# Kernel optimization log

Measured on AMD Instinct MI355X. Metric: run time of the kernel, lower is better.

The kernel has to match this reference:

```python
import jax, jax.numpy as jnp
import numpy as np

N = 50000      # nodes
E = 100000     # edges
F_NODE = 128
F_EDGE = 16
H = 64         # hidden_dim
OUT = 32
STEPS = 3
G = 64         # num_graphs (static; batch.max()+1 in torch)


def setup_inputs() -> dict:
    key = jax.random.key(0)
    ks = jax.random.split(key, 20)

    def lin(k, fin, fout):
        s = 1.0 / np.sqrt(fin)
        return jax.random.uniform(k, (fin, fout), jnp.float32, -s, s)

    def bias(k, fin, fout):
        s = 1.0 / np.sqrt(fin)
        return jax.random.uniform(k, (fout,), jnp.float32, -s, s)

    inp = {
        'x': jax.random.normal(ks[0], (N, F_NODE), jnp.float32),
        'edge_index': jax.random.randint(ks[1], (2, E), 0, N),
        'edge_attr': jax.random.normal(ks[2], (E, F_EDGE), jnp.float32),
        'batch': jnp.sort(jax.random.randint(ks[3], (N,), 0, G)),
        # node encoder
        'W_enc': lin(ks[4], F_NODE, H), 'b_enc': bias(ks[5], F_NODE, H),
        # edge_nn: Linear(F_EDGE,H) -> ReLU -> Linear(H, H*H)
        'W_e1': lin(ks[6], F_EDGE, H), 'b_e1': bias(ks[7], F_EDGE, H),
        'W_e2': lin(ks[8], H, H * H), 'b_e2': bias(ks[9], H, H * H),
        # GRUCell (torch layout: [3H, H])
        'W_ih': jax.random.uniform(ks[10], (3 * H, H), jnp.float32, -1/np.sqrt(H), 1/np.sqrt(H)),
        'W_hh': jax.random.uniform(ks[11], (3 * H, H), jnp.float32, -1/np.sqrt(H), 1/np.sqrt(H)),
        'b_ih': jax.random.uniform(ks[12], (3 * H,), jnp.float32, -1/np.sqrt(H), 1/np.sqrt(H)),
        'b_hh': jax.random.uniform(ks[13], (3 * H,), jnp.float32, -1/np.sqrt(H), 1/np.sqrt(H)),
        # readout MLP: Linear(H,H) -> ReLU -> Linear(H,OUT)
        'W_r1': lin(ks[14], H, H), 'b_r1': bias(ks[15], H, H),
        'W_r2': lin(ks[16], H, OUT), 'b_r2': bias(ks[17], H, OUT),
    }
    return inp


def gru_cell(m, h, W_ih, W_hh, b_ih, b_hh):
    gi = m @ W_ih.T + b_ih   # [N, 3H]
    gh = h @ W_hh.T + b_hh
    i_r, i_z, i_n = jnp.split(gi, 3, axis=-1)
    h_r, h_z, h_n = jnp.split(gh, 3, axis=-1)
    r = jax.nn.sigmoid(i_r + h_r)
    z = jax.nn.sigmoid(i_z + h_z)
    n = jnp.tanh(i_n + r * h_n)
    return (1.0 - z) * n + z * h


def reference(x, edge_index, edge_attr, batch, W_enc, b_enc, W_e1, b_e1,
              W_e2, b_e2, W_ih, W_hh, b_ih, b_hh, W_r1, b_r1, W_r2, b_r2):
    h = x @ W_enc + b_enc                                   # [N, H]
    src, dst = edge_index[0], edge_index[1]
    # edge-conditioned weight matrices (loop-invariant; compute once)
    ew = (jax.nn.relu(edge_attr @ W_e1 + b_e1) @ W_e2 + b_e2).reshape(E, H, H)
    for _ in range(STEPS):
        msg = jnp.einsum('eij,ej->ei', ew, h[src])          # per-edge matvec
        m_agg = jax.ops.segment_sum(msg, dst, num_segments=N)
        h = gru_cell(m_agg, h, W_ih, W_hh, b_ih, b_hh)
    g = jax.ops.segment_sum(h, batch, num_segments=G)       # sum readout
    return jax.nn.relu(g @ W_r1 + b_r1) @ W_r2 + b_r2
```

## Files before the change

kernel.cpp:

```cpp
#include <hip/hip_runtime.h>
#include <hip/hip_bf16.h>
#include <math.h>

#define NN 50000
#define NE 100000
#define FN 128
#define FE 16
#define HD 64
#define OUTD 32
#define NG 64
#define ZK 65

typedef unsigned int uint;
typedef unsigned short ushort;
typedef __attribute__((ext_vector_type(8))) short short8;
typedef __attribute__((ext_vector_type(16))) float f32x16;

static __device__ __forceinline__ float bfbits2f(uint u) {
    return __builtin_bit_cast(float, u << 16);
}
static __device__ __forceinline__ uint packbf(float f0, float f1) {
    return __builtin_amdgcn_perm(__builtin_bit_cast(uint, f1),
                                 __builtin_bit_cast(uint, f0), 0x07060302u);
}
static __device__ __forceinline__ ushort f2bf(float f) {
    uint u = __builtin_bit_cast(uint, f);
    u = (u + 0x7FFFu + ((u >> 16) & 1u)) >> 16;
    return (ushort)u;
}
static __device__ __forceinline__ uint pack2rne(float f0, float f1) {
    return (uint)f2bf(f0) | ((uint)f2bf(f1) << 16);
}
static __device__ __forceinline__ float fsigmoid(float x) {
    return 1.f / (1.f + __expf(-x));
}
static __device__ __forceinline__ float ftanh(float x) {
    float t = __expf(2.f * x);
    return 1.f - 2.f / (t + 1.f);
}

#define PREP_S0 (ZK * 4096)
#define PREP_S1 (256 * 128)
__global__ void k_prep(const float* __restrict__ W_e2, const float* __restrict__ b_e2,
                       const float* __restrict__ W_ih, const float* __restrict__ W_hh,
                       ushort* __restrict__ Wtb, ushort* __restrict__ Bg) {
    int idx = blockIdx.x * 256 + threadIdx.x;
    if (idx < PREP_S0) {
        int k0 = idx >> 12, r = idx & 4095;
        int jb = r >> 9, i = (r >> 3) & 63, q = r & 7;
        int j = jb * 8 + q;
        float v = (k0 < 64) ? W_e2[k0 * 4096 + i * 64 + j] : b_e2[i * 64 + j];
        Wtb[idx] = f2bf(v);
        return;
    }
    idx -= PREP_S0;
    if (idx < PREP_S1) {
        int n = idx >> 7, k = idx & 127;
        int g = n >> 6, i = n & 63;
        float v = 0.f;
        if (g == 0)      v = (k < 64) ? W_ih[i * 64 + k]         : W_hh[i * 64 + (k - 64)];
        else if (g == 1) v = (k < 64) ? W_ih[(64 + i) * 64 + k]  : W_hh[(64 + i) * 64 + (k - 64)];
        else if (g == 2) v = (k < 64) ? W_ih[(128 + i) * 64 + k] : 0.f;
        else             v = (k < 64) ? 0.f                      : W_hh[(128 + i) * 64 + (k - 64)];
        Bg[idx] = f2bf(v);
    }
}

#define NBENC ((NN + 127) / 128)
#define NBEDG ((NE + 255) / 256)
__global__ __launch_bounds__(256, 2)
void k_enc_edge(const float* __restrict__ x, const float* __restrict__ W_enc,
                const float* __restrict__ b_enc,
                const float* __restrict__ ea, const float* __restrict__ W_e1,
                const float* __restrict__ b_e1,
                ushort* __restrict__ hb, ushort* __restrict__ zbT) {
    int t = threadIdx.x;
    if (blockIdx.x < NBENC) {
        __shared__ __align__(16) ushort blds[64 * 128];
        int wave = t >> 6, lane = t & 63, l31 = lane & 31, lhi = lane >> 5;
        for (int idx = t; idx < 1024; idx += 256) {
            int n = idx >> 4, p = idx & 15;
            int ssrc = p ^ (n & 15);
            int kk = ssrc * 8;
            uint4 u;
            u.x = pack2rne(W_enc[(kk + 0) * 64 + n], W_enc[(kk + 1) * 64 + n]);
            u.y = pack2rne(W_enc[(kk + 2) * 64 + n], W_enc[(kk + 3) * 64 + n]);
            u.z = pack2rne(W_enc[(kk + 4) * 64 + n], W_enc[(kk + 5) * 64 + n]);
            u.w = pack2rne(W_enc[(kk + 6) * 64 + n], W_enc[(kk + 7) * 64 + n]);
            *(uint4*)&blds[idx * 8] = u;
        }
        int node0 = blockIdx.x * 128 + wave * 32;
        int m = node0 + l31;
        int mc = (m < NN) ? m : NN - 1;
        short8 afr[8];
        const float* xr = x + (size_t)mc * 128;
        #pragma unroll
        for (int ks = 0; ks < 8; ks++) {
            float4 v0 = *(const float4*)(xr + ks * 16 + lhi * 8);
            float4 v1 = *(const float4*)(xr + ks * 16 + lhi * 8 + 4);
            uint4 u;
            u.x = pack2rne(v0.x, v0.y); u.y = pack2rne(v0.z, v0.w);
            u.z = pack2rne(v1.x, v1.y); u.w = pack2rne(v1.z, v1.w);
            afr[ks] = __builtin_bit_cast(short8, u);
        }
        __syncthreads();
        #pragma unroll
        for (int ct = 0; ct < 2; ct++) {
            f32x16 acc = {0};
            int n = ct * 32 + l31;
            #pragma unroll
            for (int ks = 0; ks < 8; ks++) {
                int sp = (ks * 2 + lhi) ^ (n & 15);
                short8 bf = *(const short8*)&blds[n * 128 + sp * 8];
                acc = __builtin_amdgcn_mfma_f32_32x32x16_bf16(afr[ks], bf, acc, 0, 0, 0);
            }
            int o = ct * 32 + l31;
            float bias = b_enc[o];
            #pragma unroll
            for (int r = 0; r < 16; r++) {
                int row = (r & 3) + 8 * (r >> 2) + 4 * lhi;
                int node = node0 + row;
                if (node < NN) hb[node * 64 + o] = f2bf(acc[r] + bias);
            }
        }
    } else {
        __shared__ float Ws[16 * 64];
        __shared__ float b1s[64];
        for (int idx = t; idx < 1024; idx += 256) Ws[idx] = W_e1[idx];
        if (t < 64) b1s[t] = b_e1[t];
        __syncthreads();
        int e = (blockIdx.x - NBENC) * 256 + t;
        int ec = (e < NE) ? e : NE - 1;
        float eav[16];
        const float4* ep = (const float4*)(ea + ec * 16);
        #pragma unroll
        for (int q = 0; q < 4; q++) {
            float4 v = ep[q];
            eav[q * 4 + 0] = v.x; eav[q * 4 + 1] = v.y; eav[q * 4 + 2] = v.z; eav[q * 4 + 3] = v.w;
        }
        if (e >= NE) return;
        #pragma unroll 4
        for (int k = 0; k < 64; k++) {
            float acc = b1s[k];
            #pragma unroll
            for (int f = 0; f < 16; f++) acc += eav[f] * Ws[f * 64 + k];
            zbT[(size_t)k * NE + e] = f2bf(fmaxf(acc, 0.f));
        }
        zbT[(size_t)64 * NE + e] = f2bf(1.0f);
    }
}

__global__ __launch_bounds__(256, 2)
void k_message(const ushort* __restrict__ zbT, const ushort* __restrict__ hb,
               const int* __restrict__ eidx, const ushort* __restrict__ Wtb,
               float* __restrict__ m_agg) {
    __shared__ __align__(16) ushort wlds[2][2 * 4096];
    __shared__ __align__(16) ushort zlds[2304 * 8];
    __shared__ int sdst[256];

    int t = threadIdx.x;
    int wave = t >> 6, lane = t & 63;
    int l31 = lane & 31, lhi = lane >> 5;
    int eblk = blockIdx.x * 256;
    int e0 = eblk + wave * 64;

    {
        int e = eblk + t; if (e >= NE) e = NE - 1;
        sdst[t] = eidx[NE + e];
    }

    float hf[2][32];
    #pragma unroll
    for (int mt = 0; mt < 2; mt++) {
        int e = e0 + mt * 32 + l31;
        int ec = (e < NE) ? e : NE - 1;
        int s = eidx[ec];
        const ushort* hrow = hb + (size_t)s * 64;
        #pragma unroll
        for (int c = 0; c < 4; c++) {
            uint4 v = *(const uint4*)(hrow + c * 16 + lhi * 8);
            hf[mt][c * 8 + 0] = bfbits2f(v.x & 0xFFFFu); hf[mt][c * 8 + 1] = bfbits2f(v.x >> 16);
            hf[mt][c * 8 + 2] = bfbits2f(v.y & 0xFFFFu); hf[mt][c * 8 + 3] = bfbits2f(v.y >> 16);
            hf[mt][c * 8 + 4] = bfbits2f(v.z & 0xFFFFu); hf[mt][c * 8 + 5] = bfbits2f(v.z >> 16);
            hf[mt][c * 8 + 6] = bfbits2f(v.w & 0xFFFFu); hf[mt][c * 8 + 7] = bfbits2f(v.w >> 16);
        }
    }

    #pragma unroll
    for (int call = 0; call < 9; call++) {
        int slot = call * 256 + t;
        int k0 = slot >> 5; if (k0 > 64) k0 = 64;
        int p = slot & 31;
        const ushort* src = zbT + (size_t)k0 * NE + eblk + p * 8;
        __builtin_amdgcn_global_load_lds(
            (const __attribute__((address_space(1))) void*)src,
            (__attribute__((address_space(3))) void*)&zlds[(size_t)(call * 256 + wave * 64) * 8],
            16, 0, 0);
    }

    auto stagew = [&](int slab0, int buf) {
        #pragma unroll
        for (int call = 0; call < 4; call++) {
            int slot = call * 256 + t;
            int slab = slab0 + (slot >> 9);
            if (slab > 64) slab = 64;
            int w = slot & 511;
            const ushort* src = Wtb + (size_t)slab * 4096 + w * 8;
            __builtin_amdgcn_global_load_lds(
                (const __attribute__((address_space(1))) void*)src,
                (__attribute__((address_space(3))) void*)&wlds[buf][(size_t)(call * 256 + wave * 64) * 8],
                16, 0, 0);
        }
    };
    stagew(0, 0);

    f32x16 acc00 = {0}, acc01 = {0}, acc10 = {0}, acc11 = {0};

    for (int rnd = 0; rnd < 33; rnd++) {
        __syncthreads();
        int buf = rnd & 1;
        if (rnd < 32) stagew(2 * rnd + 2, buf ^ 1);
        int nk = (rnd < 32) ? 2 : 1;
        #pragma unroll 2
        for (int kk = 0; kk < nk; kk++) {
            int k0 = 2 * rnd + kk;
            float zf0 = bfbits2f((uint)zlds[k0 * 256 + wave * 64 + l31]);
            float zf1 = bfbits2f((uint)zlds[k0 * 256 + wave * 64 + 32 + l31]);
            const ushort* wb = &wlds[buf][kk * 4096];
            #pragma unroll
            for (int c = 0; c < 4; c++) {
                int jb = c * 2 + lhi;
                short8 b0 = *(const short8*)&wb[(jb * 64 + l31) * 8];
                short8 b1 = *(const short8*)&wb[(jb * 64 + 32 + l31) * 8];
                uint4 au0, au1;
                au0.x = packbf(zf0 * hf[0][c * 8 + 0], zf0 * hf[0][c * 8 + 1]);
                au0.y = packbf(zf0 * hf[0][c * 8 + 2], zf0 * hf[0][c * 8 + 3]);
                au0.z = packbf(zf0 * hf[0][c * 8 + 4], zf0 * hf[0][c * 8 + 5]);
                au0.w = packbf(zf0 * hf[0][c * 8 + 6], zf0 * hf[0][c * 8 + 7]);
                au1.x = packbf(zf1 * hf[1][c * 8 + 0], zf1 * hf[1][c * 8 + 1]);
                au1.y = packbf(zf1 * hf[1][c * 8 + 2], zf1 * hf[1][c * 8 + 3]);
                au1.z = packbf(zf1 * hf[1][c * 8 + 4], zf1 * hf[1][c * 8 + 5]);
                au1.w = packbf(zf1 * hf[1][c * 8 + 6], zf1 * hf[1][c * 8 + 7]);
                short8 a0 = __builtin_bit_cast(short8, au0);
                short8 a1 = __builtin_bit_cast(short8, au1);
                acc00 = __builtin_amdgcn_mfma_f32_32x32x16_bf16(a0, b0, acc00, 0, 0, 0);
                acc01 = __builtin_amdgcn_mfma_f32_32x32x16_bf16(a0, b1, acc01, 0, 0, 0);
                acc10 = __builtin_amdgcn_mfma_f32_32x32x16_bf16(a1, b0, acc10, 0, 0, 0);
                acc11 = __builtin_amdgcn_mfma_f32_32x32x16_bf16(a1, b1, acc11, 0, 0, 0);
            }
        }
    }

    #pragma unroll
    for (int r = 0; r < 16; r++) {
        int roff = (r & 3) + 8 * (r >> 2) + 4 * lhi;
        int eA = e0 + roff, eB = e0 + 32 + roff;
        if (eA < NE) {
            int d0 = sdst[wave * 64 + roff];
            atomicAdd(m_agg + d0 * 64 + l31,      acc00[r]);
            atomicAdd(m_agg + d0 * 64 + 32 + l31, acc01[r]);
        }
        if (eB < NE) {
            int d1 = sdst[wave * 64 + 32 + roff];
            atomicAdd(m_agg + d1 * 64 + l31,      acc10[r]);
            atomicAdd(m_agg + d1 * 64 + 32 + l31, acc11[r]);
        }
    }
}

__global__ __launch_bounds__(256, 2)
void k_gru(float* __restrict__ magg, const ushort* __restrict__ hb,
           const ushort* __restrict__ Bg, const float* __restrict__ b_ih,
           const float* __restrict__ b_hh, ushort* __restrict__ hb_out,
           const int* __restrict__ batch, float* __restrict__ g, int last) {
    __shared__ __align__(16) ushort blds[256 * 128];
    int t = threadIdx.x;
    int wave = t >> 6, lane = t & 63, l31 = lane & 31, lhi = lane >> 5;
    #pragma unroll
    for (int call = 0; call < 16; call++) {
        int slot = call * 256 + t;
        int n = slot >> 4, p = slot & 15;
        int ssrc = p ^ (n & 15);
        const ushort* src = Bg + n * 128 + ssrc * 8;
        __builtin_amdgcn_global_load_lds(
            (const __attribute__((address_space(1))) void*)src,
            (__attribute__((address_space(3))) void*)&blds[(size_t)(call * 256 + wave * 64) * 8],
            16, 0, 0);
    }
    int node0 = blockIdx.x * 128 + wave * 32;
    int m = node0 + l31;
    int mc = (m < NN) ? m : NN - 1;
    short8 afr[8];
    float* mrow = magg + (size_t)mc * 64;
    #pragma unroll
    for (int ks = 0; ks < 4; ks++) {
        float4 v0 = *(const float4*)(mrow + ks * 16 + lhi * 8);
        float4 v1 = *(const float4*)(mrow + ks * 16 + lhi * 8 + 4);
        uint4 u;
        u.x = pack2rne(v0.x, v0.y); u.y = pack2rne(v0.z, v0.w);
        u.z = pack2rne(v1.x, v1.y); u.w = pack2rne(v1.z, v1.w);
        afr[ks] = __builtin_bit_cast(short8, u);
    }
    if (!last) {
        float4 z4 = make_float4(0.f, 0.f, 0.f, 0.f);
        #pragma unroll
        for (int ks = 0; ks < 4; ks++) {
            *(float4*)(mrow + ks * 16 + lhi * 8) = z4;
            *(float4*)(mrow + ks * 16 + lhi * 8 + 4) = z4;
        }
    }
    const ushort* hrow = hb + (size_t)mc * 64;
    #pragma unroll
    for (int ks = 4; ks < 8; ks++) {
        uint4 v = *(const uint4*)(hrow + (ks - 4) * 16 + lhi * 8);
        afr[ks] = __builtin_bit_cast(short8, v);
    }
    __syncthreads();
    #pragma unroll
    for (int ct = 0; ct < 2; ct++) {
        f32x16 aR = {0}, aZ = {0}, aI = {0}, aH = {0};
        int nR = 0   + ct * 32 + l31;
        int nZ = 64  + ct * 32 + l31;
        int nI = 128 + ct * 32 + l31;
        int nH = 192 + ct * 32 + l31;
        #pragma unroll
        for (int ks = 0; ks < 8; ks++) {
            int s = ks * 2 + lhi;
            short8 a = afr[ks];
            short8 bR = *(const short8*)&blds[nR * 128 + (s ^ (nR & 15)) * 8];
            short8 bZ = *(const short8*)&blds[nZ * 128 + (s ^ (nZ & 15)) * 8];
            short8 bI = *(const short8*)&blds[nI * 128 + (s ^ (nI & 15)) * 8];
            short8 bH = *(const short8*)&blds[nH * 128 + (s ^ (nH & 15)) * 8];
            aR = __builtin_amdgcn_mfma_f32_32x32x16_bf16(a, bR, aR, 0, 0, 0);
            aZ = __builtin_amdgcn_mfma_f32_32x32x16_bf16(a, bZ, aZ, 0, 0, 0);
            aI = __builtin_amdgcn_mfma_f32_32x32x16_bf16(a, bI, aI, 0, 0, 0);
            aH = __builtin_amdgcn_mfma_f32_32x32x16_bf16(a, bH, aH, 0, 0, 0);
        }
        int i = ct * 32 + l31;
        float brv = b_ih[i] + b_hh[i];
        float bzv = b_ih[64 + i] + b_hh[64 + i];
        float biv = b_ih[128 + i];
        float bhv = b_hh[128 + i];
        #pragma unroll
        for (int r = 0; r < 16; r++) {
            int row = (r & 3) + 8 * (r >> 2) + 4 * lhi;
            int node = node0 + row;
            if (node < NN) {
                float ho = bfbits2f((uint)hb[node * 64 + i]);
                float rg = fsigmoid(aR[r] + brv);
                float zg = fsigmoid(aZ[r] + bzv);
                float ng = ftanh(aI[r] + biv + rg * (aH[r] + bhv));
                float hv = (1.f - zg) * ng + zg * ho;
                if (!last) hb_out[node * 64 + i] = f2bf(hv);
                else       atomicAdd(&g[batch[node] * 64 + i], hv);
            }
        }
    }
}

__global__ __launch_bounds__(1024)
void k_readout(const float* __restrict__ g, const float* __restrict__ W1, const float* __restrict__ b1,
               const float* __restrict__ W2, const float* __restrict__ b2, float* __restrict__ out) {
    __shared__ float gs[64 * 64];
    __shared__ float ts[64 * 64];
    int t = threadIdx.x;
    for (int idx = t; idx < 4096; idx += 1024) gs[idx] = g[idx];
    __syncthreads();
    for (int idx = t; idx < 4096; idx += 1024) {
        int r = idx >> 6, c = idx & 63;
        float acc = b1[c];
        #pragma unroll 8
        for (int k = 0; k < 64; k++) acc += gs[r * 64 + k] * W1[k * 64 + c];
        ts[idx] = fmaxf(acc, 0.f);
    }
    __syncthreads();
    for (int idx = t; idx < 2048; idx += 1024) {
        int r = idx >> 5, c = idx & 31;
        float acc = b2[c];
        #pragma unroll 8
        for (int k = 0; k < 64; k++) acc += ts[r * 64 + k] * W2[k * 32 + c];
        out[idx] = acc;
    }
}

extern "C" void kernel_launch(void* const* d_in, const int* in_sizes, int n_in,
                              void* d_out, int out_size, void* d_ws, size_t ws_size,
                              hipStream_t stream) {
    const float* x     = (const float*)d_in[0];
    const int*   ei    = (const int*)  d_in[1];
    const float* ea    = (const float*)d_in[2];
    const int*   batch = (const int*)  d_in[3];
    const float* W_enc = (const float*)d_in[4];
    const float* b_enc = (const float*)d_in[5];
    const float* W_e1  = (const float*)d_in[6];
    const float* b_e1  = (const float*)d_in[7];
    const float* W_e2  = (const float*)d_in[8];
    const float* b_e2  = (const float*)d_in[9];
    const float* W_ih  = (const float*)d_in[10];
    const float* W_hh  = (const float*)d_in[11];
    const float* b_ih  = (const float*)d_in[12];
    const float* b_hh  = (const float*)d_in[13];
    const float* W_r1  = (const float*)d_in[14];
    const float* b_r1  = (const float*)d_in[15];
    const float* W_r2  = (const float*)d_in[16];
    const float* b_r2  = (const float*)d_in[17];
    float* out = (float*)d_out;

    float* ws    = (float*)d_ws;
    float* magg  = ws;
    float* g     = magg + NN * 64;
    ushort* hb   = (ushort*)(g + NG * 64);
    ushort* hb2  = hb   + NN * 64;
    ushort* zbT  = hb2  + NN * 64;
    ushort* Wtb  = zbT  + (size_t)ZK * NE;
    ushort* Bgru = Wtb  + ZK * 4096;

    hipLaunchKernelGGL(k_prep, dim3((PREP_S0 + PREP_S1 + 255) / 256), dim3(256), 0, stream,
                       W_e2, b_e2, W_ih, W_hh, Wtb, Bgru);
    hipLaunchKernelGGL(k_enc_edge, dim3(NBENC + NBEDG), dim3(256), 0, stream,
                       x, W_enc, b_enc, ea, W_e1, b_e1, hb, zbT);
    hipMemsetAsync(magg, 0, (size_t)NN * 64 * sizeof(float), stream);
    hipMemsetAsync(g, 0, (size_t)NG * 64 * sizeof(float), stream);

    ushort* hbc = hb; ushort* hbn = hb2;
    for (int s = 0; s < 3; s++) {
        hipLaunchKernelGGL(k_message, dim3((NE + 255) / 256), dim3(256), 0, stream,
                           zbT, hbc, ei, Wtb, magg);
        hipLaunchKernelGGL(k_gru,     dim3((NN + 127) / 128), dim3(256), 0, stream,
                           magg, hbc, Bgru, b_ih, b_hh, hbn, batch, g, (s == 2) ? 1 : 0);
        ushort* tb = hbc; hbc = hbn; hbn = tb;
    }

    hipLaunchKernelGGL(k_readout, dim3(1), dim3(1024), 0, stream, g, W_r1, b_r1, W_r2, b_r2, out);
}
```

Measured before the change: 451.0 us.

## Switch intermediates to fp16 with packed multiplies and restructure message kernel tiling

All bf16 intermediates (weights, hidden states, edge features) become fp16, so the message kernel can form z*h products with packed half multiplies instead of unpacking to fp32 and repacking. The message kernel now handles 128 edges per block, with wave pairs splitting the output columns. Each wave stages its own weight slab per k step, waiting with s_waitcnt instead of block barriers. Occupancy hint raised to 3 blocks; fp16 range and round-toward-zero conversion add some accuracy risk.

```diff
diff --git a/kernel.cpp b/kernel.cpp
--- a/kernel.cpp
+++ b/kernel.cpp
@@ -13,23 +13,20 @@
 
 typedef unsigned int uint;
 typedef unsigned short ushort;
+typedef _Float16 half_t;
+typedef __attribute__((ext_vector_type(2))) _Float16 half2_t;
 typedef __attribute__((ext_vector_type(8))) short short8;
 typedef __attribute__((ext_vector_type(16))) float f32x16;
 
-static __device__ __forceinline__ float bfbits2f(uint u) {
-    return __builtin_bit_cast(float, u << 16);
-}
-static __device__ __forceinline__ uint packbf(float f0, float f1) {
-    return __builtin_amdgcn_perm(__builtin_bit_cast(uint, f1),
-                                 __builtin_bit_cast(uint, f0), 0x07060302u);
-}
-static __device__ __forceinline__ ushort f2bf(float f) {
-    uint u = __builtin_bit_cast(uint, f);
-    u = (u + 0x7FFFu + ((u >> 16) & 1u)) >> 16;
-    return (ushort)u;
-}
-static __device__ __forceinline__ uint pack2rne(float f0, float f1) {
-    return (uint)f2bf(f0) | ((uint)f2bf(f1) << 16);
+static __device__ __forceinline__ ushort f2h(float f) {
+    return __builtin_bit_cast(ushort, (half_t)f);
+}
+static __device__ __forceinline__ uint pkrtz(float a, float b) {
+    return __builtin_bit_cast(uint, __builtin_amdgcn_cvt_pkrtz(a, b));
+}
+static __device__ __forceinline__ uint pkmul(uint a, uint b) {
+    half2_t r = __builtin_bit_cast(half2_t, a) * __builtin_bit_cast(half2_t, b);
+    return __builtin_bit_cast(uint, r);
 }
 static __device__ __forceinline__ float fsigmoid(float x) {
     return 1.f / (1.f + __expf(-x));
@@ -50,7 +47,7 @@
         int jb = r >> 9, i = (r >> 3) & 63, q = r & 7;
         int j = jb * 8 + q;
         float v = (k0 < 64) ? W_e2[k0 * 4096 + i * 64 + j] : b_e2[i * 64 + j];
-        Wtb[idx] = f2bf(v);
+        Wtb[idx] = f2h(v);
         return;
     }
     idx -= PREP_S0;
@@ -62,7 +59,7 @@
         else if (g == 1) v = (k < 64) ? W_ih[(64 + i) * 64 + k]  : W_hh[(64 + i) * 64 + (k - 64)];
         else if (g == 2) v = (k < 64) ? W_ih[(128 + i) * 64 + k] : 0.f;
         else             v = (k < 64) ? 0.f                      : W_hh[(128 + i) * 64 + (k - 64)];
-        Bg[idx] = f2bf(v);
+        Bg[idx] = f2h(v);
     }
 }
 
@@ -83,10 +80,10 @@
             int ssrc = p ^ (n & 15);
             int kk = ssrc * 8;
             uint4 u;
-            u.x = pack2rne(W_enc[(kk + 0) * 64 + n], W_enc[(kk + 1) * 64 + n]);
-            u.y = pack2rne(W_enc[(kk + 2) * 64 + n], W_enc[(kk + 3) * 64 + n]);
-            u.z = pack2rne(W_enc[(kk + 4) * 64 + n], W_enc[(kk + 5) * 64 + n]);
-            u.w = pack2rne(W_enc[(kk + 6) * 64 + n], W_enc[(kk + 7) * 64 + n]);
+            u.x = pkrtz(W_enc[(kk + 0) * 64 + n], W_enc[(kk + 1) * 64 + n]);
+            u.y = pkrtz(W_enc[(kk + 2) * 64 + n], W_enc[(kk + 3) * 64 + n]);
+            u.z = pkrtz(W_enc[(kk + 4) * 64 + n], W_enc[(kk + 5) * 64 + n]);
+            u.w = pkrtz(W_enc[(kk + 6) * 64 + n], W_enc[(kk + 7) * 64 + n]);
             *(uint4*)&blds[idx * 8] = u;
         }
         int node0 = blockIdx.x * 128 + wave * 32;
@@ -99,8 +96,8 @@
             float4 v0 = *(const float4*)(xr + ks * 16 + lhi * 8);
             float4 v1 = *(const float4*)(xr + ks * 16 + lhi * 8 + 4);
             uint4 u;
-            u.x = pack2rne(v0.x, v0.y); u.y = pack2rne(v0.z, v0.w);
-            u.z = pack2rne(v1.x, v1.y); u.w = pack2rne(v1.z, v1.w);
+            u.x = pkrtz(v0.x, v0.y); u.y = pkrtz(v0.z, v0.w);
+            u.z = pkrtz(v1.x, v1.y); u.w = pkrtz(v1.z, v1.w);
             afr[ks] = __builtin_bit_cast(short8, u);
         }
         __syncthreads();
@@ -112,7 +109,7 @@
             for (int ks = 0; ks < 8; ks++) {
                 int sp = (ks * 2 + lhi) ^ (n & 15);
                 short8 bf = *(const short8*)&blds[n * 128 + sp * 8];
-                acc = __builtin_amdgcn_mfma_f32_32x32x16_bf16(afr[ks], bf, acc, 0, 0, 0);
+                acc = __builtin_amdgcn_mfma_f32_32x32x16_f16(afr[ks], bf, acc, 0, 0, 0);
             }
             int o = ct * 32 + l31;
             float bias = b_enc[o];
@@ -120,7 +117,7 @@
             for (int r = 0; r < 16; r++) {
                 int row = (r & 3) + 8 * (r >> 2) + 4 * lhi;
                 int node = node0 + row;
-                if (node < NN) hb[node * 64 + o] = f2bf(acc[r] + bias);
+                if (node < NN) hb[node * 64 + o] = f2h(acc[r] + bias);
             }
         }
     } else {
@@ -144,32 +141,33 @@
             float acc = b1s[k];
             #pragma unroll
             for (int f = 0; f < 16; f++) acc += eav[f] * Ws[f * 64 + k];
-            zbT[(size_t)k * NE + e] = f2bf(fmaxf(acc, 0.f));
-        }
-        zbT[(size_t)64 * NE + e] = f2bf(1.0f);
-    }
-}
-
-__global__ __launch_bounds__(256, 2)
+            zbT[(size_t)k * NE + e] = f2h(fmaxf(acc, 0.f));
+        }
+        zbT[(size_t)64 * NE + e] = f2h(1.0f);
+    }
+}
+
+__global__ __launch_bounds__(256, 3)
 void k_message(const ushort* __restrict__ zbT, const ushort* __restrict__ hb,
                const int* __restrict__ eidx, const ushort* __restrict__ Wtb,
                float* __restrict__ m_agg) {
-    __shared__ __align__(16) ushort wlds[2][2 * 4096];
-    __shared__ __align__(16) ushort zlds[2304 * 8];
-    __shared__ int sdst[256];
+    __shared__ __align__(16) ushort wlds[4][2][2048];
+    __shared__ __align__(16) ushort zlds[1280 * 8];
+    __shared__ int sdst[128];
 
     int t = threadIdx.x;
     int wave = t >> 6, lane = t & 63;
     int l31 = lane & 31, lhi = lane >> 5;
-    int eblk = blockIdx.x * 256;
-    int e0 = eblk + wave * 64;
-
-    {
+    int epair = wave >> 1, nt = wave & 1;
+    int eblk = blockIdx.x * 128;
+    int e0 = eblk + epair * 64;
+
+    if (t < 128) {
         int e = eblk + t; if (e >= NE) e = NE - 1;
         sdst[t] = eidx[NE + e];
     }
 
-    float hf[2][32];
+    uint4 hf[2][4];
     #pragma unroll
     for (int mt = 0; mt < 2; mt++) {
         int e = e0 + mt * 32 + l31;
@@ -177,20 +175,15 @@
         int s = eidx[ec];
         const ushort* hrow = hb + (size_t)s * 64;
         #pragma unroll
-        for (int c = 0; c < 4; c++) {
-            uint4 v = *(const uint4*)(hrow + c * 16 + lhi * 8);
-            hf[mt][c * 8 + 0] = bfbits2f(v.x & 0xFFFFu); hf[mt][c * 8 + 1] = bfbits2f(v.x >> 16);
-            hf[mt][c * 8 + 2] = bfbits2f(v.y & 0xFFFFu); hf[mt][c * 8 + 3] = bfbits2f(v.y >> 16);
-            hf[mt][c * 8 + 4] = bfbits2f(v.z & 0xFFFFu); hf[mt][c * 8 + 5] = bfbits2f(v.z >> 16);
-            hf[mt][c * 8 + 6] = bfbits2f(v.w & 0xFFFFu); hf[mt][c * 8 + 7] = bfbits2f(v.w >> 16);
-        }
-    }
-
-    #pragma unroll
-    for (int call = 0; call < 9; call++) {
+        for (int c = 0; c < 4; c++)
+            hf[mt][c] = *(const uint4*)(hrow + c * 16 + lhi * 8);
+    }
+
+    #pragma unroll
+    for (int call = 0; call < 5; call++) {
         int slot = call * 256 + t;
-        int k0 = slot >> 5; if (k0 > 64) k0 = 64;
-        int p = slot & 31;
+        int k0 = slot >> 4; if (k0 > 64) k0 = 64;
+        int p = slot & 15;
         const ushort* src = zbT + (size_t)k0 * NE + eblk + p * 8;
         __builtin_amdgcn_global_load_lds(
             (const __attribute__((address_space(1))) void*)src,
@@ -198,56 +191,48 @@
             16, 0, 0);
     }
 
-    auto stagew = [&](int slab0, int buf) {
-        #pragma unroll
-        for (int call = 0; call < 4; call++) {
-            int slot = call * 256 + t;
-            int slab = slab0 + (slot >> 9);
-            if (slab > 64) slab = 64;
-            int w = slot & 511;
-            const ushort* src = Wtb + (size_t)slab * 4096 + w * 8;
+    auto stagew = [&](int k0, int buf) {
+        #pragma unroll
+        for (int cc = 0; cc < 4; cc++) {
+            int s = cc * 64 + lane;
+            int jb = s >> 5, i5 = s & 31;
+            const ushort* src = Wtb + (size_t)k0 * 4096 + (size_t)(jb * 64 + nt * 32 + i5) * 8;
             __builtin_amdgcn_global_load_lds(
                 (const __attribute__((address_space(1))) void*)src,
-                (__attribute__((address_space(3))) void*)&wlds[buf][(size_t)(call * 256 + wave * 64) * 8],
+                (__attribute__((address_space(3))) void*)&wlds[wave][buf][cc * 512],
                 16, 0, 0);
         }
     };
     stagew(0, 0);
 
-    f32x16 acc00 = {0}, acc01 = {0}, acc10 = {0}, acc11 = {0};
-
-    for (int rnd = 0; rnd < 33; rnd++) {
-        __syncthreads();
-        int buf = rnd & 1;
-        if (rnd < 32) stagew(2 * rnd + 2, buf ^ 1);
-        int nk = (rnd < 32) ? 2 : 1;
-        #pragma unroll 2
-        for (int kk = 0; kk < nk; kk++) {
-            int k0 = 2 * rnd + kk;
-            float zf0 = bfbits2f((uint)zlds[k0 * 256 + wave * 64 + l31]);
-            float zf1 = bfbits2f((uint)zlds[k0 * 256 + wave * 64 + 32 + l31]);
-            const ushort* wb = &wlds[buf][kk * 4096];
-            #pragma unroll
-            for (int c = 0; c < 4; c++) {
-                int jb = c * 2 + lhi;
-                short8 b0 = *(const short8*)&wb[(jb * 64 + l31) * 8];
-                short8 b1 = *(const short8*)&wb[(jb * 64 + 32 + l31) * 8];
-                uint4 au0, au1;
-                au0.x = packbf(zf0 * hf[0][c * 8 + 0], zf0 * hf[0][c * 8 + 1]);
-                au0.y = packbf(zf0 * hf[0][c * 8 + 2], zf0 * hf[0][c * 8 + 3]);
-                au0.z = packbf(zf0 * hf[0][c * 8 + 4], zf0 * hf[0][c * 8 + 5]);
-                au0.w = packbf(zf0 * hf[0][c * 8 + 6], zf0 * hf[0][c * 8 + 7]);
-                au1.x = packbf(zf1 * hf[1][c * 8 + 0], zf1 * hf[1][c * 8 + 1]);
-                au1.y = packbf(zf1 * hf[1][c * 8 + 2], zf1 * hf[1][c * 8 + 3]);
-                au1.z = packbf(zf1 * hf[1][c * 8 + 4], zf1 * hf[1][c * 8 + 5]);
-                au1.w = packbf(zf1 * hf[1][c * 8 + 6], zf1 * hf[1][c * 8 + 7]);
-                short8 a0 = __builtin_bit_cast(short8, au0);
-                short8 a1 = __builtin_bit_cast(short8, au1);
-                acc00 = __builtin_amdgcn_mfma_f32_32x32x16_bf16(a0, b0, acc00, 0, 0, 0);
-                acc01 = __builtin_amdgcn_mfma_f32_32x32x16_bf16(a0, b1, acc01, 0, 0, 0);
-                acc10 = __builtin_amdgcn_mfma_f32_32x32x16_bf16(a1, b0, acc10, 0, 0, 0);
-                acc11 = __builtin_amdgcn_mfma_f32_32x32x16_bf16(a1, b1, acc11, 0, 0, 0);
-            }
+    __syncthreads();
+
+    f32x16 acc0 = {0}, acc1 = {0};
+
+    for (int k0 = 0; k0 < ZK; k0++) {
+        int buf = k0 & 1;
+        if (k0 + 1 < ZK) {
+            stagew(k0 + 1, buf ^ 1);
+            __builtin_amdgcn_s_waitcnt(0x0F74);
+        } else {
+            __builtin_amdgcn_s_waitcnt(0x0F70);
+        }
+        ushort z0 = zlds[k0 * 128 + epair * 64 + l31];
+        ushort z1 = zlds[k0 * 128 + epair * 64 + 32 + l31];
+        uint zd0 = (uint)z0 | ((uint)z0 << 16);
+        uint zd1 = (uint)z1 | ((uint)z1 << 16);
+        #pragma unroll
+        for (int c = 0; c < 4; c++) {
+            short8 b = *(const short8*)&wlds[wave][buf][(size_t)((c * 2 + lhi) * 32 + l31) * 8];
+            uint4 a0u, a1u;
+            a0u.x = pkmul(hf[0][c].x, zd0); a0u.y = pkmul(hf[0][c].y, zd0);
+            a0u.z = pkmul(hf[0][c].z, zd0); a0u.w = pkmul(hf[0][c].w, zd0);
+            a1u.x = pkmul(hf[1][c].x, zd1); a1u.y = pkmul(hf[1][c].y, zd1);
+            a1u.z = pkmul(hf[1][c].z, zd1); a1u.w = pkmul(hf[1][c].w, zd1);
+            short8 a0 = __builtin_bit_cast(short8, a0u);
+            short8 a1 = __builtin_bit_cast(short8, a1u);
+            acc0 = __builtin_amdgcn_mfma_f32_32x32x16_f16(a0, b, acc0, 0, 0, 0);
+            acc1 = __builtin_amdgcn_mfma_f32_32x32x16_f16(a1, b, acc1, 0, 0, 0);
         }
     }
 
@@ -256,14 +241,12 @@
         int roff = (r & 3) + 8 * (r >> 2) + 4 * lhi;
         int eA = e0 + roff, eB = e0 + 32 + roff;
         if (eA < NE) {
-            int d0 = sdst[wave * 64 + roff];
-            atomicAdd(m_agg + d0 * 64 + l31,      acc00[r]);
-            atomicAdd(m_agg + d0 * 64 + 32 + l31, acc01[r]);
+            int d0 = sdst[epair * 64 + roff];
+            atomicAdd(m_agg + d0 * 64 + nt * 32 + l31, acc0[r]);
         }
         if (eB < NE) {
-            int d1 = sdst[wave * 64 + 32 + roff];
-            atomicAdd(m_agg + d1 * 64 + l31,      acc10[r]);
-            atomicAdd(m_agg + d1 * 64 + 32 + l31, acc11[r]);
+            int d1 = sdst[epair * 64 + 32 + roff];
+            atomicAdd(m_agg + d1 * 64 + nt * 32 + l31, acc1[r]);
         }
     }
 }
@@ -297,8 +280,8 @@
         float4 v0 = *(const float4*)(mrow + ks * 16 + lhi * 8);
         float4 v1 = *(const float4*)(mrow + ks * 16 + lhi * 8 + 4);
         uint4 u;
-        u.x = pack2rne(v0.x, v0.y); u.y = pack2rne(v0.z, v0.w);
-        u.z = pack2rne(v1.x, v1.y); u.w = pack2rne(v1.z, v1.w);
+        u.x = pkrtz(v0.x, v0.y); u.y = pkrtz(v0.z, v0.w);
+        u.z = pkrtz(v1.x, v1.y); u.w = pkrtz(v1.z, v1.w);
         afr[ks] = __builtin_bit_cast(short8, u);
     }
     if (!last) {
@@ -331,10 +314,10 @@
             short8 bZ = *(const short8*)&blds[nZ * 128 + (s ^ (nZ & 15)) * 8];
             short8 bI = *(const short8*)&blds[nI * 128 + (s ^ (nI & 15)) * 8];
             short8 bH = *(const short8*)&blds[nH * 128 + (s ^ (nH & 15)) * 8];
-            aR = __builtin_amdgcn_mfma_f32_32x32x16_bf16(a, bR, aR, 0, 0, 0);
-            aZ = __builtin_amdgcn_mfma_f32_32x32x16_bf16(a, bZ, aZ, 0, 0, 0);
-            aI = __builtin_amdgcn_mfma_f32_32x32x16_bf16(a, bI, aI, 0, 0, 0);
-            aH = __builtin_amdgcn_mfma_f32_32x32x16_bf16(a, bH, aH, 0, 0, 0);
+            aR = __builtin_amdgcn_mfma_f32_32x32x16_f16(a, bR, aR, 0, 0, 0);
+            aZ = __builtin_amdgcn_mfma_f32_32x32x16_f16(a, bZ, aZ, 0, 0, 0);
+            aI = __builtin_amdgcn_mfma_f32_32x32x16_f16(a, bI, aI, 0, 0, 0);
+            aH = __builtin_amdgcn_mfma_f32_32x32x16_f16(a, bH, aH, 0, 0, 0);
         }
         int i = ct * 32 + l31;
         float brv = b_ih[i] + b_hh[i];
@@ -346,12 +329,12 @@
             int row = (r & 3) + 8 * (r >> 2) + 4 * lhi;
             int node = node0 + row;
             if (node < NN) {
-                float ho = bfbits2f((uint)hb[node * 64 + i]);
+                float ho = (float)__builtin_bit_cast(half_t, hb[node * 64 + i]);
                 float rg = fsigmoid(aR[r] + brv);
                 float zg = fsigmoid(aZ[r] + bzv);
                 float ng = ftanh(aI[r] + biv + rg * (aH[r] + bhv));
                 float hv = (1.f - zg) * ng + zg * ho;
-                if (!last) hb_out[node * 64 + i] = f2bf(hv);
+                if (!last) hb_out[node * 64 + i] = f2h(hv);
                 else       atomicAdd(&g[batch[node] * 64 + i], hv);
             }
         }
@@ -424,7 +407,7 @@
 
     ushort* hbc = hb; ushort* hbn = hb2;
     for (int s = 0; s < 3; s++) {
-        hipLaunchKernelGGL(k_message, dim3((NE + 255) / 256), dim3(256), 0, stream,
+        hipLaunchKernelGGL(k_message, dim3((NE + 127) / 128), dim3(256), 0, stream,
                            zbT, hbc, ei, Wtb, magg);
         hipLaunchKernelGGL(k_gru,     dim3((NN + 127) / 128), dim3(256), 0, stream,
                            magg, hbc, Bgru, b_ih, b_hh, hbn, batch, g, (s == 2) ? 1 : 0);
```

Measured after the change: 506.5 us. 1.12x slower.
